# Performance work log

Measured on AMD Instinct MI355X. Metric: run time of the kernel, lower is better.

Reference implementation:

```python
import jax, jax.numpy as jnp
import numpy as np

N_NODES = 100000
N_EDGES = 1600000
IN_F = 256
OUT_F = 128


def setup_inputs() -> dict:
    key = jax.random.key(0)
    k_x, k_r, k_c, k_v, k_w, k_b = jax.random.split(key, 6)
    x = jax.random.normal(k_x, (N_NODES, IN_F), dtype=jnp.float32)
    edge_row = jnp.sort(jax.random.randint(k_r, (N_EDGES,), 0, N_NODES, dtype=jnp.int32))
    edge_col = jax.random.randint(k_c, (N_EDGES,), 0, N_NODES, dtype=jnp.int32)
    edge_val = jax.random.uniform(k_v, (N_EDGES,), dtype=jnp.float32)
    stdv = 1.0 / np.sqrt(OUT_F)
    weight = jax.random.uniform(k_w, (IN_F, OUT_F), dtype=jnp.float32, minval=-stdv, maxval=stdv)
    bias = jax.random.uniform(k_b, (OUT_F,), dtype=jnp.float32, minval=-stdv, maxval=stdv)
    return {"x": x, "edge_row": edge_row, "edge_col": edge_col,
            "edge_val": edge_val, "weight": weight, "bias": bias}


def reference(x, edge_row, edge_col, edge_val, weight, bias):
    # support = X @ W   [N, OUT_F]
    support = x @ weight
    # output = spmm(adj, support): gather neighbor features, weight, scatter-add by row
    msgs = edge_val[:, None] * support[edge_col]  # [E, OUT_F]
    output = jax.ops.segment_sum(msgs, edge_row, num_segments=N_NODES)
    return output + bias
```

## Files before the change

kernel.cpp:

```cpp
#include <hip/hip_runtime.h>
#include <hip/hip_bf16.h>

#define N_NODES 100000
#define N_EDGES 1600000
#define IN_F 256
#define OUT_F 128

typedef __attribute__((ext_vector_type(8))) __bf16 bf16x8;
typedef __attribute__((ext_vector_type(4))) float f32x4;

__device__ __forceinline__ unsigned short f2bf(float f) {
    union { float f; unsigned int i; } u; u.f = f;
    unsigned int r = u.i + 0x7fff + ((u.i >> 16) & 1);
    return (unsigned short)(r >> 16);
}

__global__ __launch_bounds__(256) void wconv_kernel(
    const float* __restrict__ weight, unsigned short* __restrict__ wt) {
  int id = blockIdx.x * 256 + threadIdx.x;
  int col = id & 127;
  int k   = id >> 7;
  wt[(size_t)col * IN_F + k] = f2bf(weight[(size_t)k * OUT_F + col]);
}

#define XS 72
#define WSS 72
__global__ __launch_bounds__(256) void gemm_xw_mfma(
    const float* __restrict__ x, const unsigned short* __restrict__ wt,
    unsigned char* __restrict__ support_q ,
    float* __restrict__ scales ) {
  __shared__ unsigned short smem[13824];
  unsigned short* Xt = smem;
  unsigned short* Wt = smem + 4608;

  const int tid  = threadIdx.x;
  const int w    = tid >> 6;
  const int lane = tid & 63;
  const int l15  = lane & 15;
  const int lhi  = lane >> 4;
  const int row0 = blockIdx.x * 64;

  f32x4 acc[8];
  #pragma unroll
  for (int nt = 0; nt < 8; ++nt) acc[nt] = (f32x4){0.f, 0.f, 0.f, 0.f};

  for (int ks = 0; ks < 4; ++ks) {
    {
      int r = tid >> 2;
      int srow = row0 + r; if (srow >= N_NODES) srow = N_NODES - 1;
      const float* xp = x + (size_t)srow * IN_F + ks * 64;
      #pragma unroll
      for (int i = 0; i < 4; ++i) {
        int f4 = (tid & 3) + i * 4;
        float4 v = *(const float4*)(xp + f4 * 4);
        ushort4 h;
        h.x = f2bf(v.x); h.y = f2bf(v.y); h.z = f2bf(v.z); h.w = f2bf(v.w);
        *(ushort4*)(&Xt[r * XS + f4 * 4]) = h;
      }
    }
    {
      int c = tid >> 1;
      const unsigned short* wp = wt + (size_t)c * IN_F + ks * 64;
      #pragma unroll
      for (int i = 0; i < 4; ++i) {
        int c8 = (tid & 1) * 4 + i;
        uint4 v = *(const uint4*)(wp + c8 * 8);
        *(uint4*)(&Wt[c * WSS + c8 * 8]) = v;
      }
    }
    __syncthreads();
    #pragma unroll
    for (int kt = 0; kt < 2; ++kt) {
      bf16x8 a = *(const bf16x8*)(&Xt[(w * 16 + l15) * XS + kt * 32 + lhi * 8]);
      #pragma unroll
      for (int nt = 0; nt < 8; ++nt) {
        bf16x8 b = *(const bf16x8*)(&Wt[(nt * 16 + l15) * WSS + kt * 32 + lhi * 8]);
        acc[nt] = __builtin_amdgcn_mfma_f32_16x16x32_bf16(a, b, acc[nt], 0, 0, 0);
      }
    }
    __syncthreads();
  }

  float m0 = 0.f, m1 = 0.f, m2 = 0.f, m3 = 0.f;
  #pragma unroll
  for (int nt = 0; nt < 8; ++nt) {
    m0 = fmaxf(m0, fabsf(acc[nt][0]));
    m1 = fmaxf(m1, fabsf(acc[nt][1]));
    m2 = fmaxf(m2, fabsf(acc[nt][2]));
    m3 = fmaxf(m3, fabsf(acc[nt][3]));
  }
  #pragma unroll
  for (int off = 1; off <= 8; off <<= 1) {
    m0 = fmaxf(m0, __shfl_xor(m0, off, 64));
    m1 = fmaxf(m1, __shfl_xor(m1, off, 64));
    m2 = fmaxf(m2, __shfl_xor(m2, off, 64));
    m3 = fmaxf(m3, __shfl_xor(m3, off, 64));
  }
  #pragma unroll
  for (int r = 0; r < 4; ++r) {
    float m = (r == 0) ? m0 : (r == 1) ? m1 : (r == 2) ? m2 : m3;
    float inv = m > 0.f ? 127.0f / m : 0.f;
    unsigned int lo = 0, hi = 0;
    #pragma unroll
    for (int nt = 0; nt < 4; ++nt) {
      int q = (int)rintf(acc[nt][r] * inv);
      lo |= ((unsigned int)(q & 255)) << (8 * nt);
    }
    #pragma unroll
    for (int nt = 4; nt < 8; ++nt) {
      int q = (int)rintf(acc[nt][r] * inv);
      hi |= ((unsigned int)(q & 255)) << (8 * (nt - 4));
    }
    int row = row0 + w * 16 + lhi * 4 + r;
    if (row < N_NODES) {
      uint2 p; p.x = lo; p.y = hi;
      *(uint2*)(support_q + (size_t)row * 128 + l15 * 8) = p;
    }
  }
  if (l15 < 4) {
    float m = (l15 == 0) ? m0 : (l15 == 1) ? m1 : (l15 == 2) ? m2 : m3;
    int row = row0 + w * 16 + lhi * 4 + l15;
    if (row < N_NODES) scales[row] = m * (1.0f / 127.0f);
  }
}

__global__ __launch_bounds__(256) void rowptr_kernel(
    const int* __restrict__ edge_row, int* __restrict__ row_ptr) {
  int r = blockIdx.x * 256 + threadIdx.x;
  if (r > N_NODES) return;
  int lo = 0, hi = N_EDGES;
  while (lo < hi) {
    int mid = (lo + hi) >> 1;
    if (edge_row[mid] < r) lo = mid + 1; else hi = mid;
  }
  row_ptr[r] = lo;
}

__global__ __launch_bounds__(256) void spmm_kernel(
    const unsigned char* __restrict__ support_q,
    const float* __restrict__ scales,
    const int* __restrict__ row_ptr,
    const int* __restrict__ edge_col,
    const float* __restrict__ edge_val,
    const float* __restrict__ bias,
    float* __restrict__ out) {
  int row = (blockIdx.x * 256 + threadIdx.x) >> 6;
  row = __builtin_amdgcn_readfirstlane(row);
  if (row >= N_NODES) return;
  const int lane = threadIdx.x & 63;
  const int esl  = lane >> 5;
  const int fg   = lane & 31;

  const int cbase = (fg & 1) * 64 + (fg >> 1);
  const int c0o = cbase, c1o = cbase + 16, c2o = cbase + 32, c3o = cbase + 48;
  const float b0 = bias[c0o], b1 = bias[c1o], b2 = bias[c2o], b3 = bias[c3o];

  int e   = row_ptr[row];
  int end = row_ptr[row + 1];
  float a0 = 0.f, a1 = 0.f, a2 = 0.f, a3 = 0.f;

  while (e < end) {
    const int tm1 = end - 1;
#define EDGE_LD(g) \
    int   ei##g = e + 2 * g + esl; \
    int   j##g  = ei##g < end ? ei##g : tm1; \
    int   c##g  = edge_col[j##g]; \
    float v##g  = ei##g < end ? edge_val[j##g] : 0.f;
    EDGE_LD(0) EDGE_LD(1) EDGE_LD(2) EDGE_LD(3)
    EDGE_LD(4) EDGE_LD(5) EDGE_LD(6) EDGE_LD(7)
#undef EDGE_LD
#define GATH(g) \
    unsigned int s##g = *(const unsigned int*)(support_q + (size_t)c##g * 128 + fg * 4); \
    float sc##g = scales[c##g];
    GATH(0) GATH(1) GATH(2) GATH(3)
    GATH(4) GATH(5) GATH(6) GATH(7)
#undef GATH
#define ACCUM(g) { \
    float wv = v##g * sc##g; \
    a0 += wv * (float)(((int)(s##g << 24)) >> 24); \
    a1 += wv * (float)(((int)(s##g << 16)) >> 24); \
    a2 += wv * (float)(((int)(s##g <<  8)) >> 24); \
    a3 += wv * (float)(((int)s##g) >> 24); }
    ACCUM(0) ACCUM(1) ACCUM(2) ACCUM(3)
    ACCUM(4) ACCUM(5) ACCUM(6) ACCUM(7)
#undef ACCUM
    e += 16;
  }

  a0 += __shfl_xor(a0, 32, 64);
  a1 += __shfl_xor(a1, 32, 64);
  a2 += __shfl_xor(a2, 32, 64);
  a3 += __shfl_xor(a3, 32, 64);

  if (lane < 32) {
    float* op = out + (size_t)row * OUT_F;
    op[c0o] = a0 + b0;
    op[c1o] = a1 + b1;
    op[c2o] = a2 + b2;
    op[c3o] = a3 + b3;
  }
}

extern "C" void kernel_launch(void* const* d_in, const int* in_sizes, int n_in,
                              void* d_out, int out_size, void* d_ws, size_t ws_size,
                              hipStream_t stream) {
  const float* x        = (const float*)d_in[0];
  const int*   edge_row = (const int*)  d_in[1];
  const int*   edge_col = (const int*)  d_in[2];
  const float* edge_val = (const float*)d_in[3];
  const float* weight   = (const float*)d_in[4];
  const float* bias     = (const float*)d_in[5];
  float* out = (float*)d_out;

  unsigned char* ws = (unsigned char*)d_ws;
  size_t sq_bytes = (size_t)N_NODES * 128;
  unsigned char* support_q = ws;
  size_t rp_off = (sq_bytes + 255) & ~(size_t)255;
  int* row_ptr = (int*)(ws + rp_off);
  size_t wt_off = (rp_off + (size_t)(N_NODES + 1) * 4 + 255) & ~(size_t)255;
  unsigned short* wt = (unsigned short*)(ws + wt_off);
  size_t sc_off = (wt_off + (size_t)IN_F * OUT_F * 2 + 255) & ~(size_t)255;
  float* scales = (float*)(ws + sc_off);

  hipLaunchKernelGGL(rowptr_kernel, dim3((N_NODES + 1 + 255) / 256), dim3(256), 0, stream,
                     edge_row, row_ptr);
  hipLaunchKernelGGL(wconv_kernel, dim3(128), dim3(256), 0, stream,
                     weight, wt);
  hipLaunchKernelGGL(gemm_xw_mfma, dim3((N_NODES + 63) / 64), dim3(256), 0, stream,
                     x, wt, support_q, scales);
  hipLaunchKernelGGL(spmm_kernel, dim3(N_NODES / 4), dim3(256), 0, stream,
                     support_q, scales, row_ptr, edge_col, edge_val, bias, out);
}
```

Before: 87.61 us.

## Pack edge column and quantized weight into one word; integer SpMM accumulation

Adds a prep kernel that folds edge_val times the per-row scale into a 15-bit fixed-point weight and packs it with the 17-bit column index into one 32-bit word per edge. The SpMM then reads a single word per edge instead of col, val and scale, gathers 8 bytes per lane across 16 lanes, accumulates in integers, and reduces across four edge slots. This cuts gather and index traffic and float conversions, at the cost of an extra pass over the edges. It also adds quantization error and assumes nonnegative edge weights whose scaled value fits the 15-bit range.

Result: slower. 92.52 us (+5.6%).

```diff
diff --git a/kernel.cpp b/kernel.cpp
--- a/kernel.cpp
+++ b/kernel.cpp
@@ -136,68 +136,87 @@
   row_ptr[r] = lo;
 }
 
+__global__ __launch_bounds__(256) void prep_kernel(
+    const int* __restrict__ edge_col, const float* __restrict__ edge_val,
+    const float* __restrict__ scales, unsigned int* __restrict__ epack) {
+  int e = blockIdx.x * 256 + threadIdx.x;
+  if (e >= N_EDGES + 16) return;
+  if (e >= N_EDGES) { epack[e] = 0; return; }
+  int c = edge_col[e];
+  float wv = edge_val[e] * scales[c];
+  int q = (int)rintf(wv * 524288.0f);
+  q = q > 32767 ? 32767 : q;
+  q = q < 0 ? 0 : q;
+  epack[e] = (unsigned int)c | ((unsigned int)q << 17);
+}
+
 __global__ __launch_bounds__(256) void spmm_kernel(
     const unsigned char* __restrict__ support_q,
-    const float* __restrict__ scales,
+    const unsigned int* __restrict__ epack,
     const int* __restrict__ row_ptr,
-    const int* __restrict__ edge_col,
-    const float* __restrict__ edge_val,
     const float* __restrict__ bias,
     float* __restrict__ out) {
   int row = (blockIdx.x * 256 + threadIdx.x) >> 6;
   row = __builtin_amdgcn_readfirstlane(row);
   if (row >= N_NODES) return;
   const int lane = threadIdx.x & 63;
-  const int esl  = lane >> 5;
-  const int fg   = lane & 31;
-
-  const int cbase = (fg & 1) * 64 + (fg >> 1);
-  const int c0o = cbase, c1o = cbase + 16, c2o = cbase + 32, c3o = cbase + 48;
-  const float b0 = bias[c0o], b1 = bias[c1o], b2 = bias[c2o], b3 = bias[c3o];
-
-  int e   = row_ptr[row];
-  int end = row_ptr[row + 1];
-  float a0 = 0.f, a1 = 0.f, a2 = 0.f, a3 = 0.f;
-
-  while (e < end) {
-    const int tm1 = end - 1;
-#define EDGE_LD(g) \
-    int   ei##g = e + 2 * g + esl; \
-    int   j##g  = ei##g < end ? ei##g : tm1; \
-    int   c##g  = edge_col[j##g]; \
-    float v##g  = ei##g < end ? edge_val[j##g] : 0.f;
-    EDGE_LD(0) EDGE_LD(1) EDGE_LD(2) EDGE_LD(3)
-    EDGE_LD(4) EDGE_LD(5) EDGE_LD(6) EDGE_LD(7)
-#undef EDGE_LD
+  const int esl  = lane >> 4;
+  const int fg   = lane & 15;
+
+  float b0 = bias[fg], b1 = bias[16 + fg], b2 = bias[32 + fg], b3 = bias[48 + fg];
+  float b4 = bias[64 + fg], b5 = bias[80 + fg], b6 = bias[96 + fg], b7 = bias[112 + fg];
+
+  int e = row_ptr[row];
+  int t = row_ptr[row + 1];
+
+  int a0 = 0, a1 = 0, a2 = 0, a3 = 0, a4 = 0, a5 = 0, a6 = 0, a7 = 0;
+
+  while (e < t) {
+    const unsigned int* eb = epack + e + esl;
+    unsigned int p0 = eb[0];
+    unsigned int p1 = eb[4];
+    unsigned int p2 = eb[8];
+    unsigned int p3 = eb[12];
+    int el = e + esl;
+#define UNP(g) \
+    unsigned int c##g = p##g & 0x1FFFFu; \
+    int wq##g = (el + 4 * g < t) ? (int)((p##g >> 17) & 0x7FFFu) : 0;
+    UNP(0) UNP(1) UNP(2) UNP(3)
+#undef UNP
 #define GATH(g) \
-    unsigned int s##g = *(const unsigned int*)(support_q + (size_t)c##g * 128 + fg * 4); \
-    float sc##g = scales[c##g];
+    uint2 s##g = *(const uint2*)(support_q + (size_t)(c##g * 128u + (unsigned)fg * 8u));
     GATH(0) GATH(1) GATH(2) GATH(3)
-    GATH(4) GATH(5) GATH(6) GATH(7)
 #undef GATH
-#define ACCUM(g) { \
-    float wv = v##g * sc##g; \
-    a0 += wv * (float)(((int)(s##g << 24)) >> 24); \
-    a1 += wv * (float)(((int)(s##g << 16)) >> 24); \
-    a2 += wv * (float)(((int)(s##g <<  8)) >> 24); \
-    a3 += wv * (float)(((int)s##g) >> 24); }
-    ACCUM(0) ACCUM(1) ACCUM(2) ACCUM(3)
-    ACCUM(4) ACCUM(5) ACCUM(6) ACCUM(7)
-#undef ACCUM
+#define ACC(g) { \
+    int sx = (int)s##g.x, sy = (int)s##g.y; \
+    a0 += wq##g * ((sx << 24) >> 24); \
+    a1 += wq##g * ((sx << 16) >> 24); \
+    a2 += wq##g * ((sx <<  8) >> 24); \
+    a3 += wq##g * ( sx        >> 24); \
+    a4 += wq##g * ((sy << 24) >> 24); \
+    a5 += wq##g * ((sy << 16) >> 24); \
+    a6 += wq##g * ((sy <<  8) >> 24); \
+    a7 += wq##g * ( sy        >> 24); }
+    ACC(0) ACC(1) ACC(2) ACC(3)
+#undef ACC
     e += 16;
   }
 
-  a0 += __shfl_xor(a0, 32, 64);
-  a1 += __shfl_xor(a1, 32, 64);
-  a2 += __shfl_xor(a2, 32, 64);
-  a3 += __shfl_xor(a3, 32, 64);
-
-  if (lane < 32) {
-    float* op = out + (size_t)row * OUT_F;
-    op[c0o] = a0 + b0;
-    op[c1o] = a1 + b1;
-    op[c2o] = a2 + b2;
-    op[c3o] = a3 + b3;
+#define RED(a) a += __shfl_xor(a, 16, 64); a += __shfl_xor(a, 32, 64);
+  RED(a0) RED(a1) RED(a2) RED(a3) RED(a4) RED(a5) RED(a6) RED(a7)
+#undef RED
+
+  if (lane < 16) {
+    const float S = 1.0f / 524288.0f;
+    float* op = out + (size_t)row * OUT_F + fg;
+    op[0]   = (float)a0 * S + b0;
+    op[16]  = (float)a1 * S + b1;
+    op[32]  = (float)a2 * S + b2;
+    op[48]  = (float)a3 * S + b3;
+    op[64]  = (float)a4 * S + b4;
+    op[80]  = (float)a5 * S + b5;
+    op[96]  = (float)a6 * S + b6;
+    op[112] = (float)a7 * S + b7;
   }
 }
 
@@ -221,6 +240,8 @@
   unsigned short* wt = (unsigned short*)(ws + wt_off);
   size_t sc_off = (wt_off + (size_t)IN_F * OUT_F * 2 + 255) & ~(size_t)255;
   float* scales = (float*)(ws + sc_off);
+  size_t ep_off = (sc_off + (size_t)N_NODES * 4 + 255) & ~(size_t)255;
+  unsigned int* epack = (unsigned int*)(ws + ep_off);
 
   hipLaunchKernelGGL(rowptr_kernel, dim3((N_NODES + 1 + 255) / 256), dim3(256), 0, stream,
                      edge_row, row_ptr);
@@ -228,6 +249,8 @@
                      weight, wt);
   hipLaunchKernelGGL(gemm_xw_mfma, dim3((N_NODES + 63) / 64), dim3(256), 0, stream,
                      x, wt, support_q, scales);
+  hipLaunchKernelGGL(prep_kernel, dim3((N_EDGES + 16 + 255) / 256), dim3(256), 0, stream,
+                     edge_col, edge_val, scales, epack);
   hipLaunchKernelGGL(spmm_kernel, dim3(N_NODES / 4), dim3(256), 0, stream,
-                     support_q, scales, row_ptr, edge_col, edge_val, bias, out);
-}
+                     support_q, epack, row_ptr, bias, out);
+}
```

## Split quantized support into column-half slabs and run SpMM in two phases

Applied to the files above, without the earlier changes.

The GEMM now writes the int8 support matrix as two 64-byte-per-row slabs, one per half of the output columns, instead of a single 128-byte row. The SpMM runs as two launches, one per slab, and each wavefront now handles 4 edges per step across 16 feature lanes. The aim is to halve the gather working set in each phase so more of it stays in cache. In exchange, edge_col, edge_val, scales and row_ptr are read twice, and there is an extra kernel launch.

New measurement: 110.5 us. 26.1% more time.

```diff
diff --git a/kernel.cpp b/kernel.cpp
--- a/kernel.cpp
+++ b/kernel.cpp
@@ -27,7 +27,8 @@
 #define WSS 72
 __global__ __launch_bounds__(256) void gemm_xw_mfma(
     const float* __restrict__ x, const unsigned short* __restrict__ wt,
-    unsigned char* __restrict__ support_q ,
+    unsigned char* __restrict__ slabA ,
+    unsigned char* __restrict__ slabB ,
     float* __restrict__ scales ) {
   __shared__ unsigned short smem[13824];
   unsigned short* Xt = smem;
@@ -113,8 +114,8 @@
     }
     int row = row0 + w * 16 + lhi * 4 + r;
     if (row < N_NODES) {
-      uint2 p; p.x = lo; p.y = hi;
-      *(uint2*)(support_q + (size_t)row * 128 + l15 * 8) = p;
+      *(unsigned int*)(slabA + (size_t)row * 64 + l15 * 4) = lo;
+      *(unsigned int*)(slabB + (size_t)row * 64 + l15 * 4) = hi;
     }
   }
   if (l15 < 4) {
@@ -136,68 +137,65 @@
   row_ptr[r] = lo;
 }
 
-__global__ __launch_bounds__(256) void spmm_kernel(
-    const unsigned char* __restrict__ support_q,
+__global__ __launch_bounds__(256) void spmm_phase_kernel(
+    const unsigned char* __restrict__ slab,
     const float* __restrict__ scales,
     const int* __restrict__ row_ptr,
     const int* __restrict__ edge_col,
     const float* __restrict__ edge_val,
     const float* __restrict__ bias,
-    float* __restrict__ out) {
+    float* __restrict__ out, int coff ) {
   int row = (blockIdx.x * 256 + threadIdx.x) >> 6;
   row = __builtin_amdgcn_readfirstlane(row);
   if (row >= N_NODES) return;
   const int lane = threadIdx.x & 63;
-  const int esl  = lane >> 5;
-  const int fg   = lane & 31;
-
-  const int cbase = (fg & 1) * 64 + (fg >> 1);
-  const int c0o = cbase, c1o = cbase + 16, c2o = cbase + 32, c3o = cbase + 48;
-  const float b0 = bias[c0o], b1 = bias[c1o], b2 = bias[c2o], b3 = bias[c3o];
-
-  int e   = row_ptr[row];
-  int end = row_ptr[row + 1];
+  const int esl  = lane >> 4;
+  const int fg   = lane & 15;
+
+  const float b0 = bias[coff + fg],      b1 = bias[coff + 16 + fg];
+  const float b2 = bias[coff + 32 + fg], b3 = bias[coff + 48 + fg];
+
+  int e = row_ptr[row];
+  int t = row_ptr[row + 1];
   float a0 = 0.f, a1 = 0.f, a2 = 0.f, a3 = 0.f;
 
-  while (e < end) {
-    const int tm1 = end - 1;
+  while (e < t) {
+    const int tm1 = t - 1;
 #define EDGE_LD(g) \
-    int   ei##g = e + 2 * g + esl; \
-    int   j##g  = ei##g < end ? ei##g : tm1; \
+    int   ei##g = e + esl + 4 * g; \
+    int   j##g  = ei##g < t ? ei##g : tm1; \
     int   c##g  = edge_col[j##g]; \
-    float v##g  = ei##g < end ? edge_val[j##g] : 0.f;
+    float v##g  = ei##g < t ? edge_val[j##g] : 0.f;
     EDGE_LD(0) EDGE_LD(1) EDGE_LD(2) EDGE_LD(3)
-    EDGE_LD(4) EDGE_LD(5) EDGE_LD(6) EDGE_LD(7)
 #undef EDGE_LD
+    float sc0 = scales[c0], sc1 = scales[c1];
+    float sc2 = scales[c2], sc3 = scales[c3];
 #define GATH(g) \
-    unsigned int s##g = *(const unsigned int*)(support_q + (size_t)c##g * 128 + fg * 4); \
-    float sc##g = scales[c##g];
+    unsigned int s##g = *(const unsigned int*)(slab + (size_t)c##g * 64 + fg * 4);
     GATH(0) GATH(1) GATH(2) GATH(3)
-    GATH(4) GATH(5) GATH(6) GATH(7)
 #undef GATH
-#define ACCUM(g) { \
-    float wv = v##g * sc##g; \
-    a0 += wv * (float)(((int)(s##g << 24)) >> 24); \
-    a1 += wv * (float)(((int)(s##g << 16)) >> 24); \
-    a2 += wv * (float)(((int)(s##g <<  8)) >> 24); \
-    a3 += wv * (float)(((int)s##g) >> 24); }
-    ACCUM(0) ACCUM(1) ACCUM(2) ACCUM(3)
-    ACCUM(4) ACCUM(5) ACCUM(6) ACCUM(7)
-#undef ACCUM
+#define ACC(g) { \
+    float wv = v##g * sc##g; int s = (int)s##g; \
+    a0 += wv * (float)((s << 24) >> 24); \
+    a1 += wv * (float)((s << 16) >> 24); \
+    a2 += wv * (float)((s <<  8) >> 24); \
+    a3 += wv * (float)( s        >> 24); }
+    ACC(0) ACC(1) ACC(2) ACC(3)
+#undef ACC
     e += 16;
   }
 
-  a0 += __shfl_xor(a0, 32, 64);
-  a1 += __shfl_xor(a1, 32, 64);
-  a2 += __shfl_xor(a2, 32, 64);
-  a3 += __shfl_xor(a3, 32, 64);
-
-  if (lane < 32) {
-    float* op = out + (size_t)row * OUT_F;
-    op[c0o] = a0 + b0;
-    op[c1o] = a1 + b1;
-    op[c2o] = a2 + b2;
-    op[c3o] = a3 + b3;
+  a0 += __shfl_xor(a0, 16, 64); a0 += __shfl_xor(a0, 32, 64);
+  a1 += __shfl_xor(a1, 16, 64); a1 += __shfl_xor(a1, 32, 64);
+  a2 += __shfl_xor(a2, 16, 64); a2 += __shfl_xor(a2, 32, 64);
+  a3 += __shfl_xor(a3, 16, 64); a3 += __shfl_xor(a3, 32, 64);
+
+  if (lane < 16) {
+    float* op = out + (size_t)row * OUT_F + coff + fg;
+    op[0]  = a0 + b0;
+    op[16] = a1 + b1;
+    op[32] = a2 + b2;
+    op[48] = a3 + b3;
   }
 }
 
@@ -213,9 +211,10 @@
   float* out = (float*)d_out;
 
   unsigned char* ws = (unsigned char*)d_ws;
-  size_t sq_bytes = (size_t)N_NODES * 128;
-  unsigned char* support_q = ws;
-  size_t rp_off = (sq_bytes + 255) & ~(size_t)255;
+  size_t slab_bytes = (size_t)N_NODES * 64;
+  unsigned char* slabA = ws;
+  unsigned char* slabB = ws + ((slab_bytes + 255) & ~(size_t)255);
+  size_t rp_off = 2 * ((slab_bytes + 255) & ~(size_t)255);
   int* row_ptr = (int*)(ws + rp_off);
   size_t wt_off = (rp_off + (size_t)(N_NODES + 1) * 4 + 255) & ~(size_t)255;
   unsigned short* wt = (unsigned short*)(ws + wt_off);
@@ -227,7 +226,9 @@
   hipLaunchKernelGGL(wconv_kernel, dim3(128), dim3(256), 0, stream,
                      weight, wt);
   hipLaunchKernelGGL(gemm_xw_mfma, dim3((N_NODES + 63) / 64), dim3(256), 0, stream,
-                     x, wt, support_q, scales);
-  hipLaunchKernelGGL(spmm_kernel, dim3(N_NODES / 4), dim3(256), 0, stream,
-                     support_q, scales, row_ptr, edge_col, edge_val, bias, out);
-}
+                     x, wt, slabA, slabB, scales);
+  hipLaunchKernelGGL(spmm_phase_kernel, dim3(N_NODES / 4), dim3(256), 0, stream,
+                     slabA, scales, row_ptr, edge_col, edge_val, bias, out, 0);
+  hipLaunchKernelGGL(spmm_phase_kernel, dim3(N_NODES / 4), dim3(256), 0, stream,
+                     slabB, scales, row_ptr, edge_col, edge_val, bias, out, 64);
+}
```
